# Kernel tuning notes

Hardware: AMD Instinct MI355X
Metric: run time of the kernel (lower is better)

The kernel has to match this reference:

```python
import jax, jax.numpy as jnp
import numpy as np

B, L, D = 2, 2048, 1024
H, DK, DV = 16, 64, 64
SCALE = DK ** 0.5


def setup_inputs() -> dict:
    key = jax.random.key(0)
    ks = jax.random.split(key, 7)
    s = 0.02
    return {
        "key": jax.random.normal(ks[0], (B, L, D), jnp.float32),
        "value": jax.random.normal(ks[1], (B, L, D), jnp.float32),
        "query": jax.random.normal(ks[2], (B, L, D), jnp.float32),
        # torch nn.Linear weights: [out_features, in_features]
        "wq": jax.random.normal(ks[3], (H * DK, D), jnp.float32) * s,
        "wk": jax.random.normal(ks[4], (H * DK, D), jnp.float32) * s,
        "wv": jax.random.normal(ks[5], (H * DV, D), jnp.float32) * s,
        "wo": jax.random.normal(ks[6], (D, H * DV), jnp.float32) * s,
    }


def reference(key, value, query, wq, wk, wv, wo):
    # projections (y = x @ W^T), then split heads: [B, L, H*d] -> [B, H, L, d]
    q = (query @ wq.T).reshape(B, L, H, DK).transpose(0, 2, 1, 3)
    k = (key @ wk.T).reshape(B, L, H, DK).transpose(0, 2, 1, 3)
    v = (value @ wv.T).reshape(B, L, H, DV).transpose(0, 2, 1, 3)
    # scaled dot-product attention (full score matrix, as in the original)
    scores = jnp.einsum("bhqd,bhkd->bhqk", q, k) / SCALE
    attn = jax.nn.softmax(scores, axis=-1)  # dropout p=0.0 -> identity
    ctx = jnp.einsum("bhqk,bhkd->bhqd", attn, v)
    # merge heads and final projection
    out = ctx.transpose(0, 2, 1, 3).reshape(B, L, H * DV) @ wo.T
    return out, attn
```

## Files before the change

### kernel.cpp

```cpp
#include <hip/hip_runtime.h>


typedef unsigned short u16;
typedef unsigned int   u32;
typedef __attribute__((ext_vector_type(4))) float f32x4;
typedef __attribute__((ext_vector_type(8))) u16   u16x8;
typedef __attribute__((ext_vector_type(4))) u16   u16x4;
typedef __attribute__((ext_vector_type(8))) __bf16 bf16x8;

#define MFMA16(a, b, c) __builtin_amdgcn_mfma_f32_16x16x32_bf16((a), (b), (c), 0, 0, 0)
#define VMCNT0 asm volatile("s_waitcnt vmcnt(0)" ::: "memory")
#define VMCNT4 asm volatile("s_waitcnt vmcnt(4)" ::: "memory")
#define LGKM0  asm volatile("s_waitcnt lgkmcnt(0)" ::: "memory")
#define SCHED0 __builtin_amdgcn_sched_barrier(0)
#define RAWBAR __builtin_amdgcn_s_barrier()

#if defined(__has_builtin)
#if __has_builtin(__builtin_amdgcn_global_load_lds)
#define HAS_GLL 1
#endif
#if __has_builtin(__builtin_amdgcn_exp2f)
#define EXP2(x) __builtin_amdgcn_exp2f(x)
#endif
#endif
#ifndef HAS_GLL
#define HAS_GLL 0
#endif
#ifndef EXP2
#define EXP2(x) __expf((x) * 0.69314718056f)
#endif

#define QSCALE 0.18033688011116f

__device__ __forceinline__ u16 f2bf(float x) {
    u32 u = __builtin_bit_cast(u32, x);
    u += 0x7fffu + ((u >> 16) & 1u);
    return (u16)(u >> 16);
}
__device__ __forceinline__ float bf2f(u16 x) {
    u32 u = ((u32)x) << 16;
    return __builtin_bit_cast(float, u);
}
__device__ __forceinline__ bf16x8 ld8(const u16* p) {
    return __builtin_bit_cast(bf16x8, *(const u16x8*)p);
}

__device__ __forceinline__ void stage16(const u16* g, u16* lds_base, int lane) {
#if HAS_GLL
    (void)lane;
    __builtin_amdgcn_global_load_lds(
        (const __attribute__((address_space(1))) u32*)g,
        (__attribute__((address_space(3))) u32*)lds_base, 16, 0, 0);
#else
    *(u16x8*)((char*)lds_base + lane * 16) = *(const u16x8*)g;
#endif
}

__global__ __launch_bounds__(256) void cvt_w(
    const float* __restrict__ wq, const float* __restrict__ wk,
    const float* __restrict__ wv, const float* __restrict__ wo,
    u16* __restrict__ wqb, u16* __restrict__ wkb,
    u16* __restrict__ wvb, u16* __restrict__ wob) {
    int bid = blockIdx.x;
    const float* src; u16* dst; int base;
    if      (bid < 1024) { src = wq; dst = wqb; base = bid; }
    else if (bid < 2048) { src = wk; dst = wkb; base = bid - 1024; }
    else if (bid < 3072) { src = wv; dst = wvb; base = bid - 2048; }
    else                 { src = wo; dst = wob; base = bid - 3072; }
    int i = (base * 256 + threadIdx.x) * 4;
    float4 v = *(const float4*)(src + i);
    u16x4 h = { f2bf(v.x), f2bf(v.y), f2bf(v.z), f2bf(v.w) };
    *(u16x4*)(dst + i) = h;
}

__global__ __launch_bounds__(256)
void k_qkv(const float* __restrict__ qa, const float* __restrict__ ka,
           const float* __restrict__ va,
           const u16* __restrict__ wqp, const u16* __restrict__ wkp,
           const u16* __restrict__ wvp,
           u16* __restrict__ qo, u16* __restrict__ ko, u16* __restrict__ vTo) {
    constexpr int K = 1024;
    __shared__ u16 act_lds[2][128][32];
    __shared__ u16 w_lds[2][128][32];

    const int tid = threadIdx.x, lane = tid & 63, w = tid >> 6;
    const int wr = w >> 1, wc = w & 1, lr = lane & 15, g0 = lane >> 4;
    const int bid0 = blockIdx.x;
    const int kk = bid0 / 96, gg = bid0 % 96;
    const int wgid = gg * 8 + kk;
    const int region = wgid >> 8, r = wgid & 255;
    const int act_r0 = (r >> 3) * 128, w_r0 = (r & 7) * 128;

    const float* actp = region == 0 ? qa : region == 1 ? ka : va;
    const u16*   wp   = region == 0 ? wqp : region == 1 ? wkp : wvp;

    const int srow = lane >> 2;
    const int scol = ((lane & 3) ^ ((lane >> 3) & 3)) * 8;
    const int arow = tid >> 1, ac0 = (tid & 1) * 16, lg0 = (tid & 1) * 2;
    const int apg0 = ((lg0)     ^ ((arow >> 1) & 3)) * 8;
    const int apg1 = ((lg0 + 1) ^ ((arow >> 1) & 3)) * 8;
    const int aph = (g0 ^ ((lr >> 1) & 3)) * 8;

    auto stage = [&](int kt, int buf) {
        #pragma unroll
        for (int c = 0; c < 2; ++c) {
            int rb = w * 16 + c * 64;
            stage16(wp + (size_t)(w_r0 + rb + srow) * K + kt * 32 + scol,
                    &w_lds[buf][rb][0], lane);
        }
        const float* as = actp + (size_t)(act_r0 + arow) * K + kt * 32 + ac0;
        f32x4 v0 = *(const f32x4*)as;
        f32x4 v1 = *(const f32x4*)(as + 4);
        f32x4 v2 = *(const f32x4*)(as + 8);
        f32x4 v3 = *(const f32x4*)(as + 12);
        u16x8 h0 = { f2bf(v0[0]), f2bf(v0[1]), f2bf(v0[2]), f2bf(v0[3]),
                     f2bf(v1[0]), f2bf(v1[1]), f2bf(v1[2]), f2bf(v1[3]) };
        u16x8 h1 = { f2bf(v2[0]), f2bf(v2[1]), f2bf(v2[2]), f2bf(v2[3]),
                     f2bf(v3[0]), f2bf(v3[1]), f2bf(v3[2]), f2bf(v3[3]) };
        *(u16x8*)&act_lds[buf][arow][apg0] = h0;
        *(u16x8*)&act_lds[buf][arow][apg1] = h1;
    };

    f32x4 acc[4][4] = {};
    stage(0, 0);
    VMCNT0;
    __syncthreads();

    for (int kt = 0; kt < 32; ++kt) {
        if (kt + 1 < 32) stage(kt + 1, (kt + 1) & 1);
        const int buf = kt & 1;
        const u16 (*ml)[32] = (region < 2) ? act_lds[buf] : w_lds[buf];
        const u16 (*nl)[32] = (region < 2) ? w_lds[buf]   : act_lds[buf];
        bf16x8 mf[4], nf[4];
        #pragma unroll
        for (int m = 0; m < 4; ++m) mf[m] = ld8(&ml[wr * 64 + m * 16 + lr][aph]);
        #pragma unroll
        for (int n = 0; n < 4; ++n) nf[n] = ld8(&nl[wc * 64 + n * 16 + lr][aph]);
        #pragma unroll
        for (int m = 0; m < 4; ++m)
            #pragma unroll
            for (int n = 0; n < 4; ++n)
                acc[m][n] = MFMA16(mf[m], nf[n], acc[m][n]);
        VMCNT0;
        __syncthreads();
    }

    const float sc = (region == 0) ? QSCALE : 1.0f;
    if (region < 2) {
        u16* dst = region == 0 ? qo : ko;
        #pragma unroll
        for (int m = 0; m < 4; ++m)
            #pragma unroll
            for (int n = 0; n < 4; ++n)
                #pragma unroll
                for (int rr = 0; rr < 4; ++rr) {
                    int grow = act_r0 + wr * 64 + m * 16 + g0 * 4 + rr;
                    int gcol = w_r0 + wc * 64 + n * 16 + lr;
                    size_t di = (size_t)((grow >> 11) * 16 + (gcol >> 6)) * 131072
                              + (size_t)(grow & 2047) * 64 + (gcol & 63);
                    dst[di] = f2bf(acc[m][n][rr] * sc);
                }
    } else {
        #pragma unroll
        for (int m = 0; m < 4; ++m)
            #pragma unroll
            for (int n = 0; n < 4; ++n)
                #pragma unroll
                for (int rr = 0; rr < 4; ++rr) {
                    int dvi = w_r0 + wr * 64 + m * 16 + g0 * 4 + rr;
                    int li  = act_r0 + wc * 64 + n * 16 + lr;
                    vTo[(size_t)dvi * 4096 + li] = f2bf(acc[m][n][rr]);
                }
    }
}

__global__ __launch_bounds__(256)
void k_out(const u16* __restrict__ A, const u16* __restrict__ Bw,
           float* __restrict__ C) {
    constexpr int K = 1024;
    __shared__ u16 a_lds[2][128][32];
    __shared__ u16 b_lds[2][64][32];

    const int tid = threadIdx.x, lane = tid & 63, w = tid >> 6;
    const int wr = w >> 1, wc = w & 1, lr = lane & 15, g0 = lane >> 4;
    const int bid = blockIdx.x;
    const int m0 = (bid & 31) * 128, n0 = (bid >> 5) * 64;

    const int srow = lane >> 2;
    const int scol = ((lane & 3) ^ ((lane >> 3) & 3)) * 8;
    const int aph = (g0 ^ ((lr >> 1) & 3)) * 8;

    auto stage = [&](int kt, int buf) {
        #pragma unroll
        for (int c = 0; c < 2; ++c) {
            int rb = w * 16 + c * 64;
            stage16(A + (size_t)(m0 + rb + srow) * K + kt * 32 + scol,
                    &a_lds[buf][rb][0], lane);
        }
        int rb2 = w * 16;
        stage16(Bw + (size_t)(n0 + rb2 + srow) * K + kt * 32 + scol,
                &b_lds[buf][rb2][0], lane);
    };

    f32x4 acc[4][2] = {};
    stage(0, 0);
    VMCNT0;
    __syncthreads();

    for (int kt = 0; kt < 32; ++kt) {
        if (kt + 1 < 32) stage(kt + 1, (kt + 1) & 1);
        const int buf = kt & 1;
        bf16x8 mf[4], nf[2];
        #pragma unroll
        for (int m = 0; m < 4; ++m) mf[m] = ld8(&a_lds[buf][wr * 64 + m * 16 + lr][aph]);
        #pragma unroll
        for (int n = 0; n < 2; ++n) nf[n] = ld8(&b_lds[buf][wc * 32 + n * 16 + lr][aph]);
        #pragma unroll
        for (int m = 0; m < 4; ++m)
            #pragma unroll
            for (int n = 0; n < 2; ++n)
                acc[m][n] = MFMA16(mf[m], nf[n], acc[m][n]);
        VMCNT0;
        __syncthreads();
    }

    #pragma unroll
    for (int m = 0; m < 4; ++m)
        #pragma unroll
        for (int n = 0; n < 2; ++n)
            #pragma unroll
            for (int rr = 0; rr < 4; ++rr) {
                int grow = m0 + wr * 64 + m * 16 + g0 * 4 + rr;
                int gcol = n0 + wc * 32 + n * 16 + lr;
                C[(size_t)grow * 1024 + gcol] = acc[m][n][rr];
            }
}

__global__ __launch_bounds__(256, 4)
void attn_kernel(const u16* __restrict__ qw, const u16* __restrict__ kw,
                 const u16* __restrict__ vT, float* __restrict__ attn_o,
                 u16* __restrict__ ctx_o) {
    constexpr int L = 2048;
    __shared__ __attribute__((aligned(16))) char smem[33792];
    typedef u16 K1Row[64];
    K1Row* k1b0 = (K1Row*)smem;
    K1Row* k1b1 = (K1Row*)(smem + 16384);
    K1Row* k2b0 = (K1Row*)smem;
    K1Row* k2b1 = (K1Row*)(smem + 8192);
    K1Row* vt   = (K1Row*)(smem + 16384);
    typedef u16 PRow[72];
    PRow* pl = (PRow*)(smem + 24576);

    const int tid = threadIdx.x, w = tid >> 6, lane = tid & 63;
    const int bid = blockIdx.x;
    const int bh = (bid & 7) + 8 * (bid >> 8);
    const int qb = (bid >> 3) & 31;
    const int b = bh >> 4, h = bh & 15;
    const int qr0 = qb * 64 + w * 16;
    const int lr = lane & 15, g0 = lane >> 4;

    const u16* kbh = kw + (size_t)bh * L * 64;
    const u16* vbh = vT + (size_t)(h * 64) * 4096 + b * 2048;

    const int srow8 = lane >> 3;
    const int scol8 = ((lane & 7) ^ srow8) * 8;
    const int kph0 = (g0 ^ (lr & 7)) * 8;
    const int kph1 = ((g0 + 4) ^ (lr & 7)) * 8;

    size_t qbase = ((size_t)bh * L + qr0 + lr) * 64 + g0 * 8;
    bf16x8 aq0 = ld8(qw + qbase);
    bf16x8 aq1 = ld8(qw + qbase + 32);

    PRow* plw = pl + w * 16;

    auto stageK1 = [&](int kv, K1Row* dst) {
        #pragma unroll
        for (int c = 0; c < 4; ++c) {
            int rb = c * 32 + w * 8;
            stage16(kbh + (size_t)(kv + rb + srow8) * 64 + scol8, &dst[rb][0], lane);
        }
    };
    float ssum = 0.f;
    stageK1(0, k1b0);
    VMCNT0;
    __syncthreads();
    for (int t = 0; t < 16; ++t) {
        if (t + 1 < 16) stageK1((t + 1) * 128, (t & 1) ? k1b0 : k1b1);
        K1Row* kb = (t & 1) ? k1b1 : k1b0;
        f32x4 sacc[8] = {};
        #pragma unroll
        for (int n = 0; n < 8; ++n) {
            const u16* krow = &kb[n * 16 + lr][0];
            sacc[n] = MFMA16(ld8(krow + kph0), aq0, sacc[n]);
            sacc[n] = MFMA16(ld8(krow + kph1), aq1, sacc[n]);
        }
        #pragma unroll
        for (int n = 0; n < 8; ++n)
            #pragma unroll
            for (int rr = 0; rr < 4; ++rr)
                ssum += EXP2(sacc[n][rr]);
        VMCNT0;
        __syncthreads();
    }
    ssum += __shfl_xor(ssum, 16);
    ssum += __shfl_xor(ssum, 32);
    const float rinv = 1.f / ssum;

    auto stageK = [&](int kv, K1Row* dst) {
        #pragma unroll
        for (int c = 0; c < 2; ++c) {
            int rb = c * 32 + w * 8;
            stage16(kbh + (size_t)(kv + rb + srow8) * 64 + scol8, &dst[rb][0], lane);
        }
    };
    auto stageV = [&](int kv) {
        #pragma unroll
        for (int c = 0; c < 2; ++c) {
            int rb = w * 16 + c * 8;
            stage16(vbh + (size_t)(rb + srow8) * 4096 + kv + scol8, &vt[rb][0], lane);
        }
    };

    f32x4 cacc[4] = {};
    float* attn_b = attn_o + (size_t)bh * L * L;
    stageK(0, k2b0);
    VMCNT0;
    __syncthreads();

    for (int t = 0; t < 32; ++t) {
        const int kv = t * 64;
        K1Row* kb = (t & 1) ? k2b1 : k2b0;
        stageV(kv);
        if (t + 1 < 32) stageK(kv + 64, (t & 1) ? k2b0 : k2b1);
        SCHED0;
        if (t > 0) {
            const int kvp = kv - 64;
            #pragma unroll
            for (int rep = 0; rep < 4; ++rep) {
                int row = rep * 4 + g0;
                u16x4 pv4 = *(const u16x4*)&plw[row][lr * 4];
                f32x4 f0 = { bf2f(pv4[0]), bf2f(pv4[1]), bf2f(pv4[2]), bf2f(pv4[3]) };
                __builtin_nontemporal_store(
                    f0, (f32x4*)(attn_b + (size_t)(qr0 + row) * L + kvp + lr * 4));
            }
        }
        f32x4 sacc[4] = {};
        #pragma unroll
        for (int n = 0; n < 4; ++n) {
            const u16* krow = &kb[n * 16 + lr][0];
            sacc[n] = MFMA16(ld8(krow + kph0), aq0, sacc[n]);
            sacc[n] = MFMA16(ld8(krow + kph1), aq1, sacc[n]);
        }
        if (t == 0) { VMCNT0; } else { VMCNT4; }
        SCHED0; RAWBAR; SCHED0;

        #pragma unroll
        for (int n = 0; n < 4; ++n) {
            float p0 = EXP2(sacc[n][0]) * rinv;
            float p1 = EXP2(sacc[n][1]) * rinv;
            float p2 = EXP2(sacc[n][2]) * rinv;
            float p3 = EXP2(sacc[n][3]) * rinv;
            u16x4 pk = { f2bf(p0), f2bf(p1), f2bf(p2), f2bf(p3) };
            *(u16x4*)&plw[lr][n * 16 + g0 * 4] = pk;
        }
        #pragma unroll
        for (int kk = 0; kk < 2; ++kk) {
            bf16x8 ap = ld8(&plw[lr][kk * 32 + g0 * 8]);
            const int vph = ((kk * 4 + g0) ^ (lr & 7)) * 8;
            #pragma unroll
            for (int n2 = 0; n2 < 4; ++n2) {
                bf16x8 bv = ld8(&vt[n2 * 16 + lr][vph]);
                cacc[n2] = MFMA16(ap, bv, cacc[n2]);
            }
        }
        LGKM0;
        SCHED0; RAWBAR; SCHED0;
    }
    #pragma unroll
    for (int rep = 0; rep < 4; ++rep) {
        int row = rep * 4 + g0;
        u16x4 pv4 = *(const u16x4*)&plw[row][lr * 4];
        f32x4 f0 = { bf2f(pv4[0]), bf2f(pv4[1]), bf2f(pv4[2]), bf2f(pv4[3]) };
        __builtin_nontemporal_store(
            f0, (f32x4*)(attn_b + (size_t)(qr0 + row) * L + (L - 64) + lr * 4));
    }

    #pragma unroll
    for (int n2 = 0; n2 < 4; ++n2)
        #pragma unroll
        for (int rr = 0; rr < 4; ++rr)
            ctx_o[((size_t)b * L + qr0 + g0 * 4 + rr) * 1024 + h * 64 + n2 * 16 + lr]
                = f2bf(cacc[n2][rr]);
}

extern "C" void kernel_launch(void* const* d_in, const int* in_sizes, int n_in,
                              void* d_out, int out_size, void* d_ws, size_t ws_size,
                              hipStream_t stream) {
    const float* key   = (const float*)d_in[0];
    const float* value = (const float*)d_in[1];
    const float* query = (const float*)d_in[2];
    const float* wq    = (const float*)d_in[3];
    const float* wk    = (const float*)d_in[4];
    const float* wv    = (const float*)d_in[5];
    const float* wo    = (const float*)d_in[6];

    char* ws = (char*)d_ws;
    const size_t MB = 1024 * 1024;
    u16* wq_b = (u16*)(ws + 0 * MB);
    u16* wk_b = (u16*)(ws + 2 * MB);
    u16* wv_b = (u16*)(ws + 4 * MB);
    u16* wo_b = (u16*)(ws + 6 * MB);
    u16* q_b  = (u16*)(ws + 8 * MB);
    u16* k_b  = (u16*)(ws + 16 * MB);
    u16* vT_b = (u16*)(ws + 24 * MB);
    u16* ctx_b= (u16*)(ws + 32 * MB);

    cvt_w<<<4096, 256, 0, stream>>>(wq, wk, wv, wo, wq_b, wk_b, wv_b, wo_b);

    k_qkv<<<768, 256, 0, stream>>>(query, key, value, wq_b, wk_b, wv_b,
                                   q_b, k_b, vT_b);

    float* attn_out = (float*)d_out + 4194304;
    attn_kernel<<<dim3(1024), 256, 0, stream>>>(q_b, k_b, vT_b, attn_out, ctx_b);

    k_out<<<dim3(512), 256, 0, stream>>>(ctx_b, wo_b, (float*)d_out);
}
```

Measured before the change: 195.8 us.

## Double-buffer V tiles in attention loop and drop the mid-iteration barrier

The V^T tile gets its own pair of LDS buffers. The next iteration's K and V tiles are now prefetched together one step ahead, so the barrier and vmcnt wait that used to sit between the QK^T MFMAs and the softmax/PV phase are removed. Each iteration keeps a single wait and barrier at its end. LDS per block grows and launch bounds drop from 4 to 3 blocks per CU, trading occupancy for more registers and fewer synchronisation stalls.

```diff
diff --git a/kernel.cpp b/kernel.cpp
--- a/kernel.cpp
+++ b/kernel.cpp
@@ -11,7 +11,6 @@
 #define MFMA16(a, b, c) __builtin_amdgcn_mfma_f32_16x16x32_bf16((a), (b), (c), 0, 0, 0)
 #define VMCNT0 asm volatile("s_waitcnt vmcnt(0)" ::: "memory")
 #define VMCNT4 asm volatile("s_waitcnt vmcnt(4)" ::: "memory")
-#define LGKM0  asm volatile("s_waitcnt lgkmcnt(0)" ::: "memory")
 #define SCHED0 __builtin_amdgcn_sched_barrier(0)
 #define RAWBAR __builtin_amdgcn_s_barrier()
 
@@ -236,20 +235,21 @@
             }
 }
 
-__global__ __launch_bounds__(256, 4)
+__global__ __launch_bounds__(256, 3)
 void attn_kernel(const u16* __restrict__ qw, const u16* __restrict__ kw,
                  const u16* __restrict__ vT, float* __restrict__ attn_o,
                  u16* __restrict__ ctx_o) {
     constexpr int L = 2048;
-    __shared__ __attribute__((aligned(16))) char smem[33792];
-    typedef u16 K1Row[64];
-    K1Row* k1b0 = (K1Row*)smem;
-    K1Row* k1b1 = (K1Row*)(smem + 16384);
-    K1Row* k2b0 = (K1Row*)smem;
-    K1Row* k2b1 = (K1Row*)(smem + 8192);
-    K1Row* vt   = (K1Row*)(smem + 16384);
+    __shared__ __attribute__((aligned(16))) char smem[41984];
+    typedef u16 KRow[64];
+    KRow* k1b0 = (KRow*)smem;
+    KRow* k1b1 = (KRow*)(smem + 16384);
+    KRow* k2b0 = (KRow*)smem;
+    KRow* k2b1 = (KRow*)(smem + 8192);
+    KRow* vtb0 = (KRow*)(smem + 16384);
+    KRow* vtb1 = (KRow*)(smem + 24576);
     typedef u16 PRow[72];
-    PRow* pl = (PRow*)(smem + 24576);
+    PRow* pl = (PRow*)(smem + 32768);
 
     const int tid = threadIdx.x, w = tid >> 6, lane = tid & 63;
     const int bid = blockIdx.x;
@@ -273,7 +273,7 @@
 
     PRow* plw = pl + w * 16;
 
-    auto stageK1 = [&](int kv, K1Row* dst) {
+    auto stageK1 = [&](int kv, KRow* dst) {
         #pragma unroll
         for (int c = 0; c < 4; ++c) {
             int rb = c * 32 + w * 8;
@@ -286,7 +286,7 @@
     __syncthreads();
     for (int t = 0; t < 16; ++t) {
         if (t + 1 < 16) stageK1((t + 1) * 128, (t & 1) ? k1b0 : k1b1);
-        K1Row* kb = (t & 1) ? k1b1 : k1b0;
+        KRow* kb = (t & 1) ? k1b1 : k1b0;
         f32x4 sacc[8] = {};
         #pragma unroll
         for (int n = 0; n < 8; ++n) {
@@ -306,32 +306,36 @@
     ssum += __shfl_xor(ssum, 32);
     const float rinv = 1.f / ssum;
 
-    auto stageK = [&](int kv, K1Row* dst) {
+    auto stageK = [&](int kv, KRow* dst) {
         #pragma unroll
         for (int c = 0; c < 2; ++c) {
             int rb = c * 32 + w * 8;
             stage16(kbh + (size_t)(kv + rb + srow8) * 64 + scol8, &dst[rb][0], lane);
         }
     };
-    auto stageV = [&](int kv) {
+    auto stageV = [&](int kv, KRow* dst) {
         #pragma unroll
         for (int c = 0; c < 2; ++c) {
             int rb = w * 16 + c * 8;
-            stage16(vbh + (size_t)(rb + srow8) * 4096 + kv + scol8, &vt[rb][0], lane);
+            stage16(vbh + (size_t)(rb + srow8) * 4096 + kv + scol8, &dst[rb][0], lane);
         }
     };
 
     f32x4 cacc[4] = {};
     float* attn_b = attn_o + (size_t)bh * L * L;
     stageK(0, k2b0);
+    stageV(0, vtb0);
     VMCNT0;
     __syncthreads();
 
     for (int t = 0; t < 32; ++t) {
-        const int kv = t * 64;
-        K1Row* kb = (t & 1) ? k2b1 : k2b0;
-        stageV(kv);
-        if (t + 1 < 32) stageK(kv + 64, (t & 1) ? k2b0 : k2b1);
+        const int kv = t * 64, buf = t & 1;
+        KRow* kcur = buf ? k2b1 : k2b0;
+        KRow* vcur = buf ? vtb1 : vtb0;
+        if (t + 1 < 32) {
+            stageV(kv + 64, buf ? vtb0 : vtb1);
+            stageK(kv + 64, buf ? k2b0 : k2b1);
+        }
         SCHED0;
         if (t > 0) {
             const int kvp = kv - 64;
@@ -347,13 +351,10 @@
         f32x4 sacc[4] = {};
         #pragma unroll
         for (int n = 0; n < 4; ++n) {
-            const u16* krow = &kb[n * 16 + lr][0];
+            const u16* krow = &kcur[n * 16 + lr][0];
             sacc[n] = MFMA16(ld8(krow + kph0), aq0, sacc[n]);
             sacc[n] = MFMA16(ld8(krow + kph1), aq1, sacc[n]);
         }
-        if (t == 0) { VMCNT0; } else { VMCNT4; }
-        SCHED0; RAWBAR; SCHED0;
-
         #pragma unroll
         for (int n = 0; n < 4; ++n) {
             float p0 = EXP2(sacc[n][0]) * rinv;
@@ -369,11 +370,11 @@
             const int vph = ((kk * 4 + g0) ^ (lr & 7)) * 8;
             #pragma unroll
             for (int n2 = 0; n2 < 4; ++n2) {
-                bf16x8 bv = ld8(&vt[n2 * 16 + lr][vph]);
+                bf16x8 bv = ld8(&vcur[n2 * 16 + lr][vph]);
                 cacc[n2] = MFMA16(ap, bv, cacc[n2]);
             }
         }
-        LGKM0;
+        if (t == 0) { VMCNT0; } else { VMCNT4; }
         SCHED0; RAWBAR; SCHED0;
     }
     #pragma unroll
```

New measurement: 195.1 us. Within noise of the previous version (-0.3%).
